# Kernel optimization log

Hardware: AMD Instinct MI355X
Metric: run time of the kernel (lower is better)

Reference implementation:

```python
import jax, jax.numpy as jnp
import numpy as np

L = 5  # history window (init kwarg)

def _mlp(x, W1, b1, W2, b2, W3, b3):
    h = jax.nn.relu(x @ W1 + b1)
    h = jax.nn.relu(h @ W2 + b2)
    return h @ W3 + b3

def setup_inputs() -> dict:
    key = jax.random.key(0)
    ks = jax.random.split(key, 12)
    N, T1, S, D, H, E = 2000, 11, 5, 64, 256, 100000
    IN = 2 * D + 2 * L * S + 3 + 1 + 1  # 183
    return {
        "features": jax.random.normal(ks[0], (N, D), jnp.float32),
        "states": jax.random.uniform(ks[1], (N, T1, S), jnp.float32),
        "distances": jax.random.uniform(ks[2], (N, N), jnp.float32),
        "W1": jax.random.normal(ks[3], (IN, H), jnp.float32) * 0.05,
        "b1": jnp.zeros((H,), jnp.float32),
        "W2": jax.random.normal(ks[4], (H, H), jnp.float32) * 0.05,
        "b2": jnp.zeros((H,), jnp.float32),
        "W3": jax.random.normal(ks[5], (H, 3), jnp.float32) * 0.05,
        "b3": jnp.zeros((3,), jnp.float32),
        "pairs_i": jax.random.randint(ks[6], (E,), 0, N, jnp.int32),
        "pairs_j": jax.random.randint(ks[7], (E,), 0, N, jnp.int32),
        "max_timestep": 10,
    }

def reference(features, states, distances, W1, b1, W2, b2, W3, b3, pairs_i, pairs_j, max_timestep):
    T = int(max_timestep)  # static
    N, T1, S = states.shape
    E = pairs_i.shape[0]
    # --- state histories: hist[t, n] = states[n, max(0,t-L+1)..t] zero-padded, flattened to L*S
    pad = jnp.pad(states, ((0, 0), (L - 1, 0), (0, 0)))  # [N, T1+L-1, S]
    idx = jnp.arange(T + 1)[:, None] + jnp.arange(L)[None, :]  # [T+1, L]
    hist = pad[:, idx, :]  # [N, T+1, L, S]
    hist = jnp.transpose(hist, (1, 0, 2, 3)).reshape(T + 1, N, L * S)
    hist = jax.lax.stop_gradient(hist)  # original .detach()

    fi = features[pairs_i]              # [E, D]
    fj = features[pairs_j]              # [E, D]
    dist = distances[pairs_i, pairs_j][:, None]  # [E, 1]
    eye3 = jnp.eye(3, dtype=features.dtype)

    # --- t = 0: is_initial=1, dummy prev type = onehot(0); same conditional for all k_prev
    x0 = jnp.concatenate([
        fi, fj, hist[0, pairs_i], hist[0, pairs_j],
        jnp.broadcast_to(eye3[0], (E, 3)), dist, jnp.ones_like(dist)
    ], axis=-1)
    p0 = jax.nn.softmax(_mlp(x0, W1, b1, W2, b2, W3, b3), axis=-1)  # [E, 3]
    cond0 = jnp.broadcast_to(p0[:, None, :], (E, 3, 3))              # [E, 3, 3]
    m0 = p0

    # --- t >= 1: one NN call on 3 stacked prev-type branches, then forward-algo recursion
    hp_i = hist[1:, pairs_i]  # [T, E, L*S]
    hp_j = hist[1:, pairs_j]
    prev3 = jnp.broadcast_to(eye3[:, None, :], (3, E, 3))
    tail = jnp.concatenate([dist, jnp.zeros_like(dist)], axis=-1)  # [E, 2] (dist, is_initial=0)

    def step(m_prev, xs):
        hi, hj = xs
        base = jnp.concatenate([fi, fj, hi, hj], axis=-1)  # [E, 2D+2LS]
        x = jnp.concatenate([
            jnp.broadcast_to(base[None], (3, E, base.shape[-1])),
            prev3,
            jnp.broadcast_to(tail[None], (3, E, 2)),
        ], axis=-1)  # [3, E, IN]
        probs = jax.nn.softmax(_mlp(x, W1, b1, W2, b2, W3, b3), axis=-1)  # [3, E, 3]
        cond = jnp.transpose(probs, (1, 0, 2))  # [E, k_prev, k_next]
        m = jnp.einsum('ek,ekn->en', m_prev, cond)
        return m, (cond, m)

    _, (conds, margs) = jax.lax.scan(step, m0, (hp_i, hp_j))
    conditionals = jnp.concatenate([cond0[None], conds], axis=0)  # [T+1, E, 3, 3]
    marginals = jnp.concatenate([m0[None], margs], axis=0)        # [T+1, E, 3]
    return conditionals, marginals
```

## Files before the change

kernel.cpp:

```cpp
#include <hip/hip_runtime.h>
#include <hip/hip_bf16.h>
#include <math.h>

#define D_F   64
#define IN_F  183
#define KS1   6
#define KS2   8
#define HID   256
#define HPITCH 264
#define BM    64
#define BLK   512

typedef unsigned short u16;
typedef __attribute__((ext_vector_type(8))) short bf16x8;
typedef __attribute__((ext_vector_type(4))) float f32x4;

__device__ __forceinline__ u16 f2bf(float v) {
    __hip_bfloat16 h = __float2bfloat16(v);
    u16 u; __builtin_memcpy(&u, &h, 2); return u;
}

__global__ void pack_w_kernel(const float* __restrict__ W, u16* __restrict__ Wp,
                              int K, int KSs)
{
    int g = blockIdx.x * 256 + threadIdx.x;
    int total = 16 * KSs * 64;
    if (g >= total) return;
    int lane = g & 63;
    int ks   = (g >> 6) % KSs;
    int mt   = (g >> 6) / KSs;
    int col  = mt * 16 + (lane & 15);
    int kb   = ks * 32 + 8 * (lane >> 4);
    u16 out[8];
    #pragma unroll
    for (int j = 0; j < 8; ++j) {
        int k = kb + j;
        out[j] = f2bf((k < K) ? W[(size_t)k * HID + col] : 0.0f);
    }
    *(bf16x8*)(Wp + (size_t)g * 8) = *(const bf16x8*)out;
}

__global__ void pack_w3_kernel(const float* __restrict__ W3, u16* __restrict__ W3p)
{
    int g = blockIdx.x * 256 + threadIdx.x;
    if (g >= KS2 * 64) return;
    int lane = g & 63;
    int ks   = g >> 6;
    int n    = lane & 15;
    int kb   = ks * 32 + 8 * (lane >> 4);
    u16 out[8];
    #pragma unroll
    for (int j = 0; j < 8; ++j)
        out[j] = f2bf((n < 3) ? W3[(size_t)(kb + j) * 3 + n] : 0.0f);
    *(bf16x8*)(W3p + (size_t)g * 8) = *(const bf16x8*)out;
}

__global__ __launch_bounds__(BLK)
void mfp_mlp_mfma(const float* __restrict__ features,
                  const float* __restrict__ states,
                  const float* __restrict__ distances,
                  const float* __restrict__ W1,
                  const u16* __restrict__ W1p, const float* __restrict__ b1,
                  const u16* __restrict__ W2p, const float* __restrict__ b2,
                  const u16* __restrict__ W3p, const float* __restrict__ b3,
                  const int* __restrict__ pairs_i, const int* __restrict__ pairs_j,
                  float* __restrict__ cond,
                  int N, int T1s, int E, int T)
{
    extern __shared__ char smem[];
    u16* buf0 = (u16*)smem;
    u16* buf1 = buf0 + BM * HPITCH;
    u16* hsB  = buf1 + BM * HPITCH;
    __shared__ int   s_pi[BM], s_pj[BM], s_e[BM], s_val[BM];
    __shared__ float s_dist[BM];

    const int tid = threadIdx.x;
    const int t   = blockIdx.y;
    const int nk  = (t == 0) ? 1 : 3;

    if (tid < BM) {
        int pe = blockIdx.x * BM + tid;
        int valid = (pe < E) ? 1 : 0;
        int e = valid ? pe : 0;
        int pi = pairs_i[e], pj = pairs_j[e];
        s_e[tid] = e; s_val[tid] = valid; s_pi[tid] = pi; s_pj[tid] = pj;
        s_dist[tid] = distances[(long long)pi * N + pj];
    }
    __syncthreads();

    u16* xs = buf0;
    for (int idx = tid; idx < BM * 32; idx += BLK) {
        int m = idx >> 5;
        int q = idx & 31;
        int src = (q < 16) ? s_pi[m] : s_pj[m];
        int c4  = (q & 15) * 4;
        float4 f = *(const float4*)&features[(size_t)src * D_F + c4];
        int c = ((q < 16) ? 0 : 64) + c4;
        ushort4 o;
        o.x = f2bf(f.x); o.y = f2bf(f.y); o.z = f2bf(f.z); o.w = f2bf(f.w);
        *(ushort4*)(xs + m * HPITCH + c) = o;
    }
    for (int idx = tid; idx < BM * 64; idx += BLK) {
        int m = idx >> 6;
        int c = 128 + (idx & 63);
        float v;
        if (c < 178) {
            int cc = c - 128;
            int row = (cc < 25) ? s_pi[m] : s_pj[m];
            int c2  = (cc < 25) ? cc : (cc - 25);
            int l = c2 / 5;
            int s = c2 - l * 5;
            int tau = t - 4 + l;
            v = (tau >= 0) ? states[((size_t)row * T1s + tau) * 5 + s] : 0.0f;
        } else if (c == 181) {
            v = s_dist[m];
        } else if (c == 182) {
            v = (t == 0) ? 1.0f : 0.0f;
        } else {
            v = 0.0f;
        }
        xs[m * HPITCH + c] = f2bf(v);
    }
    __syncthreads();

    const int lane = tid & 63;
    const int w    = tid >> 6;
    const int lr   = lane & 15;
    const int lg   = lane >> 4;

    f32x4 acc1[2][4];
    #pragma unroll
    for (int a = 0; a < 2; ++a)
        #pragma unroll
        for (int b = 0; b < 4; ++b)
            acc1[a][b] = (f32x4){0.f, 0.f, 0.f, 0.f};

    for (int ks = 0; ks < KS1; ++ks) {
        bf16x8 wfr[2];
        #pragma unroll
        for (int mtl = 0; mtl < 2; ++mtl)
            wfr[mtl] = *(const bf16x8*)(W1p + (((size_t)(2 * w + mtl) * KS1 + ks) * 64 + lane) * 8);
        bf16x8 xfr[4];
        #pragma unroll
        for (int nt = 0; nt < 4; ++nt)
            xfr[nt] = *(const bf16x8*)(xs + (nt * 16 + lr) * HPITCH + ks * 32 + 8 * lg);
        #pragma unroll
        for (int mtl = 0; mtl < 2; ++mtl)
            #pragma unroll
            for (int nt = 0; nt < 4; ++nt)
                acc1[mtl][nt] = __builtin_amdgcn_mfma_f32_16x16x32_bf16(wfr[mtl], xfr[nt], acc1[mtl][nt], 0, 0, 0);
    }

    f32x4 b1q[2], b2q[2];
    #pragma unroll
    for (int mtl = 0; mtl < 2; ++mtl) {
        int h0 = 16 * (2 * w + mtl) + 4 * lg;
        b1q[mtl] = *(const f32x4*)&b1[h0];
        b2q[mtl] = *(const f32x4*)&b2[h0];
    }
    const float b30 = b3[0], b31 = b3[1], b32 = b3[2];

    __syncthreads();

    #pragma unroll
    for (int mtl = 0; mtl < 2; ++mtl) {
        int h0 = 16 * (2 * w + mtl) + 4 * lg;
        f32x4 ohq = *(const f32x4*)&W1[(size_t)178 * HID + h0];
        #pragma unroll
        for (int nt = 0; nt < 4; ++nt) {
            ushort4 p;
            p.x = f2bf(fmaxf(acc1[mtl][nt][0] + b1q[mtl][0] + ohq[0], 0.0f));
            p.y = f2bf(fmaxf(acc1[mtl][nt][1] + b1q[mtl][1] + ohq[1], 0.0f));
            p.z = f2bf(fmaxf(acc1[mtl][nt][2] + b1q[mtl][2] + ohq[2], 0.0f));
            p.w = f2bf(fmaxf(acc1[mtl][nt][3] + b1q[mtl][3] + ohq[3], 0.0f));
            *(ushort4*)(buf1 + (nt * 16 + lr) * HPITCH + h0) = p;
        }
    }
    __syncthreads();

    for (int k = 0; k < nk; ++k) {
        u16* cur = (k & 1) ? buf0 : buf1;
        u16* nxt = (k & 1) ? buf1 : buf0;

        if (k + 1 < nk) {
            #pragma unroll
            for (int mtl = 0; mtl < 2; ++mtl) {
                int h0 = 16 * (2 * w + mtl) + 4 * lg;
                f32x4 ohq = *(const f32x4*)&W1[(size_t)(178 + k + 1) * HID + h0];
                #pragma unroll
                for (int nt = 0; nt < 4; ++nt) {
                    ushort4 p;
                    p.x = f2bf(fmaxf(acc1[mtl][nt][0] + b1q[mtl][0] + ohq[0], 0.0f));
                    p.y = f2bf(fmaxf(acc1[mtl][nt][1] + b1q[mtl][1] + ohq[1], 0.0f));
                    p.z = f2bf(fmaxf(acc1[mtl][nt][2] + b1q[mtl][2] + ohq[2], 0.0f));
                    p.w = f2bf(fmaxf(acc1[mtl][nt][3] + b1q[mtl][3] + ohq[3], 0.0f));
                    *(ushort4*)(nxt + (nt * 16 + lr) * HPITCH + h0) = p;
                }
            }
        }

        f32x4 acc2[2][4];
        #pragma unroll
        for (int a = 0; a < 2; ++a)
            #pragma unroll
            for (int b = 0; b < 4; ++b)
                acc2[a][b] = (f32x4){0.f, 0.f, 0.f, 0.f};

        for (int ks = 0; ks < KS2; ++ks) {
            bf16x8 wfr[2];
            #pragma unroll
            for (int mtl = 0; mtl < 2; ++mtl)
                wfr[mtl] = *(const bf16x8*)(W2p + (((size_t)(2 * w + mtl) * KS2 + ks) * 64 + lane) * 8);
            bf16x8 hfr[4];
            #pragma unroll
            for (int nt = 0; nt < 4; ++nt)
                hfr[nt] = *(const bf16x8*)(cur + (nt * 16 + lr) * HPITCH + ks * 32 + 8 * lg);
            #pragma unroll
            for (int mtl = 0; mtl < 2; ++mtl)
                #pragma unroll
                for (int nt = 0; nt < 4; ++nt)
                    acc2[mtl][nt] = __builtin_amdgcn_mfma_f32_16x16x32_bf16(wfr[mtl], hfr[nt], acc2[mtl][nt], 0, 0, 0);
        }

        #pragma unroll
        for (int mtl = 0; mtl < 2; ++mtl) {
            int h0 = 16 * (2 * w + mtl) + 4 * lg;
            #pragma unroll
            for (int nt = 0; nt < 4; ++nt) {
                ushort4 p;
                p.x = f2bf(fmaxf(acc2[mtl][nt][0] + b2q[mtl][0], 0.0f));
                p.y = f2bf(fmaxf(acc2[mtl][nt][1] + b2q[mtl][1], 0.0f));
                p.z = f2bf(fmaxf(acc2[mtl][nt][2] + b2q[mtl][2], 0.0f));
                p.w = f2bf(fmaxf(acc2[mtl][nt][3] + b2q[mtl][3], 0.0f));
                *(ushort4*)(hsB + (nt * 16 + lr) * HPITCH + h0) = p;
            }
        }
        __syncthreads();

        if (w < 4) {
            f32x4 acc3 = (f32x4){0.f, 0.f, 0.f, 0.f};
            for (int ks = 0; ks < KS2; ++ks) {
                bf16x8 hfr = *(const bf16x8*)(hsB + (w * 16 + lr) * HPITCH + ks * 32 + 8 * lg);
                bf16x8 wfr = *(const bf16x8*)(W3p + ((size_t)(ks * 64 + lane)) * 8);
                acc3 = __builtin_amdgcn_mfma_f32_16x16x32_bf16(wfr, hfr, acc3, 0, 0, 0);
            }
            int m = 16 * w + lr;
            if (lg == 0 && s_val[m]) {
                float l0 = acc3[0] + b30;
                float l1 = acc3[1] + b31;
                float l2 = acc3[2] + b32;
                float mx = fmaxf(l0, fmaxf(l1, l2));
                float e0 = expf(l0 - mx), e1 = expf(l1 - mx), e2 = expf(l2 - mx);
                float inv = 1.0f / (e0 + e1 + e2);
                float p0 = e0 * inv, p1 = e1 * inv, p2 = e2 * inv;
                size_t base = ((size_t)t * E + s_e[m]) * 9;
                if (t == 0) {
                    #pragma unroll
                    for (int kb = 0; kb < 3; ++kb) {
                        cond[base + kb * 3 + 0] = p0;
                        cond[base + kb * 3 + 1] = p1;
                        cond[base + kb * 3 + 2] = p2;
                    }
                } else {
                    cond[base + k * 3 + 0] = p0;
                    cond[base + k * 3 + 1] = p1;
                    cond[base + k * 3 + 2] = p2;
                }
            }
        }
        __syncthreads();
    }
}

__global__ __launch_bounds__(256)
void mfp_marg_kernel(const float* __restrict__ cond,
                     float* __restrict__ marg,
                     int E, int T)
{
    int e = blockIdx.x * 256 + threadIdx.x;
    if (e >= E) return;
    const float* c0 = &cond[(size_t)e * 9];
    float m0 = c0[0], m1 = c0[1], m2 = c0[2];
    marg[(size_t)e * 3 + 0] = m0;
    marg[(size_t)e * 3 + 1] = m1;
    marg[(size_t)e * 3 + 2] = m2;
    for (int t = 1; t <= T; ++t) {
        const float* c9 = &cond[((size_t)t * E + e) * 9];
        float n0 = m0 * c9[0] + m1 * c9[3] + m2 * c9[6];
        float n1 = m0 * c9[1] + m1 * c9[4] + m2 * c9[7];
        float n2 = m0 * c9[2] + m1 * c9[5] + m2 * c9[8];
        m0 = n0; m1 = n1; m2 = n2;
        float* mo = &marg[((size_t)t * E + e) * 3];
        mo[0] = m0; mo[1] = m1; mo[2] = m2;
    }
}

extern "C" void kernel_launch(void* const* d_in, const int* in_sizes, int n_in,
                              void* d_out, int out_size, void* d_ws, size_t ws_size,
                              hipStream_t stream) {
    const float* features  = (const float*)d_in[0];
    const float* states    = (const float*)d_in[1];
    const float* distances = (const float*)d_in[2];
    const float* W1 = (const float*)d_in[3];
    const float* b1 = (const float*)d_in[4];
    const float* W2 = (const float*)d_in[5];
    const float* b2 = (const float*)d_in[6];
    const float* W3 = (const float*)d_in[7];
    const float* b3 = (const float*)d_in[8];
    const int* pairs_i = (const int*)d_in[9];
    const int* pairs_j = (const int*)d_in[10];

    const int N   = in_sizes[0] / D_F;
    const int T1s = in_sizes[1] / (N * 5);
    const int E   = in_sizes[9];
    const int T   = out_size / (12 * E) - 1;

    float* cond = (float*)d_out;
    float* marg = (float*)d_out + (size_t)(T + 1) * E * 9;

    u16* W1p = (u16*)d_ws;
    u16* W2p = W1p + 16 * KS1 * 64 * 8;
    u16* W3p = W2p + 16 * KS2 * 64 * 8;

    {
        int g1 = 16 * KS1 * 64;
        int g2 = 16 * KS2 * 64;
        int g3 = KS2 * 64;
        pack_w_kernel<<<(g1 + 255) / 256, 256, 0, stream>>>(W1, W1p, IN_F, KS1);
        pack_w_kernel<<<(g2 + 255) / 256, 256, 0, stream>>>(W2, W2p, HID, KS2);
        pack_w3_kernel<<<(g3 + 255) / 256, 256, 0, stream>>>(W3, W3p);
    }

    dim3 grid((E + BM - 1) / BM, T + 1);
    const size_t lds_bytes = (size_t)3 * BM * HPITCH * sizeof(u16);

    mfp_mlp_mfma<<<grid, BLK, lds_bytes, stream>>>(
        features, states, distances, W1, W1p, b1, W2p, b2, W3p, b3,
        pairs_i, pairs_j, cond, N, T1s, E, T);

    mfp_marg_kernel<<<(E + 255) / 256, 256, 0, stream>>>(cond, marg, E, T);
}
```

Baseline: 868.8 us.

## Precompute per-node feature projections and loop timesteps inside each block

```diff
diff --git a/kernel.cpp b/kernel.cpp
--- a/kernel.cpp
+++ b/kernel.cpp
@@ -8,6 +8,7 @@
 #define KS2   8
 #define HID   256
 #define HPITCH 264
+#define XP2   72
 #define BM    64
 #define BLK   512
 
@@ -55,14 +56,44 @@
     *(bf16x8*)(W3p + (size_t)g * 8) = *(const bf16x8*)out;
 }
 
+__global__ __launch_bounds__(256)
+void a1_kernel(const float* __restrict__ features, const float* __restrict__ W1,
+               float* __restrict__ A1, int N)
+{
+    const int side = blockIdx.y;
+    const int n0   = blockIdx.x * 16;
+    const int h    = threadIdx.x;
+    __shared__ float sf[16][D_F];
+    for (int idx = threadIdx.x; idx < 16 * D_F; idx += 256) {
+        int ni = idx >> 6, d = idx & 63;
+        int n = n0 + ni;
+        sf[ni][d] = (n < N) ? features[(size_t)n * D_F + d] : 0.0f;
+    }
+    __syncthreads();
+    float acc[16];
+    #pragma unroll
+    for (int ni = 0; ni < 16; ++ni) acc[ni] = 0.0f;
+    for (int d = 0; d < D_F; ++d) {
+        float wv = W1[(size_t)(side * D_F + d) * HID + h];
+        #pragma unroll
+        for (int ni = 0; ni < 16; ++ni)
+            acc[ni] = fmaf(sf[ni][d], wv, acc[ni]);
+    }
+    #pragma unroll
+    for (int ni = 0; ni < 16; ++ni) {
+        int n = n0 + ni;
+        if (n < N) A1[((size_t)side * N + n) * HID + h] = acc[ni];
+    }
+}
+
 __global__ __launch_bounds__(BLK)
-void mfp_mlp_mfma(const float* __restrict__ features,
-                  const float* __restrict__ states,
+void mfp_mlp_mfma(const float* __restrict__ states,
                   const float* __restrict__ distances,
                   const float* __restrict__ W1,
                   const u16* __restrict__ W1p, const float* __restrict__ b1,
                   const u16* __restrict__ W2p, const float* __restrict__ b2,
                   const u16* __restrict__ W3p, const float* __restrict__ b3,
+                  const float* __restrict__ A1,
                   const int* __restrict__ pairs_i, const int* __restrict__ pairs_j,
                   float* __restrict__ cond,
                   int N, int T1s, int E, int T)
@@ -71,12 +102,13 @@
     u16* buf0 = (u16*)smem;
     u16* buf1 = buf0 + BM * HPITCH;
     u16* hsB  = buf1 + BM * HPITCH;
+    u16* x2   = hsB  + BM * HPITCH;
     __shared__ int   s_pi[BM], s_pj[BM], s_e[BM], s_val[BM];
     __shared__ float s_dist[BM];
 
-    const int tid = threadIdx.x;
-    const int t   = blockIdx.y;
-    const int nk  = (t == 0) ? 1 : 3;
+    const int tid  = threadIdx.x;
+    const int tbeg = blockIdx.y ? 6 : 0;
+    const int tend = blockIdx.y ? 11 : 6;
 
     if (tid < BM) {
         int pe = blockIdx.x * BM + tid;
@@ -88,69 +120,11 @@
     }
     __syncthreads();
 
-    u16* xs = buf0;
-    for (int idx = tid; idx < BM * 32; idx += BLK) {
-        int m = idx >> 5;
-        int q = idx & 31;
-        int src = (q < 16) ? s_pi[m] : s_pj[m];
-        int c4  = (q & 15) * 4;
-        float4 f = *(const float4*)&features[(size_t)src * D_F + c4];
-        int c = ((q < 16) ? 0 : 64) + c4;
-        ushort4 o;
-        o.x = f2bf(f.x); o.y = f2bf(f.y); o.z = f2bf(f.z); o.w = f2bf(f.w);
-        *(ushort4*)(xs + m * HPITCH + c) = o;
-    }
-    for (int idx = tid; idx < BM * 64; idx += BLK) {
-        int m = idx >> 6;
-        int c = 128 + (idx & 63);
-        float v;
-        if (c < 178) {
-            int cc = c - 128;
-            int row = (cc < 25) ? s_pi[m] : s_pj[m];
-            int c2  = (cc < 25) ? cc : (cc - 25);
-            int l = c2 / 5;
-            int s = c2 - l * 5;
-            int tau = t - 4 + l;
-            v = (tau >= 0) ? states[((size_t)row * T1s + tau) * 5 + s] : 0.0f;
-        } else if (c == 181) {
-            v = s_dist[m];
-        } else if (c == 182) {
-            v = (t == 0) ? 1.0f : 0.0f;
-        } else {
-            v = 0.0f;
-        }
-        xs[m * HPITCH + c] = f2bf(v);
-    }
-    __syncthreads();
-
     const int lane = tid & 63;
     const int w    = tid >> 6;
     const int lr   = lane & 15;
     const int lg   = lane >> 4;
 
-    f32x4 acc1[2][4];
-    #pragma unroll
-    for (int a = 0; a < 2; ++a)
-        #pragma unroll
-        for (int b = 0; b < 4; ++b)
-            acc1[a][b] = (f32x4){0.f, 0.f, 0.f, 0.f};
-
-    for (int ks = 0; ks < KS1; ++ks) {
-        bf16x8 wfr[2];
-        #pragma unroll
-        for (int mtl = 0; mtl < 2; ++mtl)
-            wfr[mtl] = *(const bf16x8*)(W1p + (((size_t)(2 * w + mtl) * KS1 + ks) * 64 + lane) * 8);
-        bf16x8 xfr[4];
-        #pragma unroll
-        for (int nt = 0; nt < 4; ++nt)
-            xfr[nt] = *(const bf16x8*)(xs + (nt * 16 + lr) * HPITCH + ks * 32 + 8 * lg);
-        #pragma unroll
-        for (int mtl = 0; mtl < 2; ++mtl)
-            #pragma unroll
-            for (int nt = 0; nt < 4; ++nt)
-                acc1[mtl][nt] = __builtin_amdgcn_mfma_f32_16x16x32_bf16(wfr[mtl], xfr[nt], acc1[mtl][nt], 0, 0, 0);
-    }
-
     f32x4 b1q[2], b2q[2];
     #pragma unroll
     for (int mtl = 0; mtl < 2; ++mtl) {
@@ -160,115 +134,168 @@
     }
     const float b30 = b3[0], b31 = b3[1], b32 = b3[2];
 
-    __syncthreads();
-
-    #pragma unroll
-    for (int mtl = 0; mtl < 2; ++mtl) {
-        int h0 = 16 * (2 * w + mtl) + 4 * lg;
-        f32x4 ohq = *(const f32x4*)&W1[(size_t)178 * HID + h0];
-        #pragma unroll
-        for (int nt = 0; nt < 4; ++nt) {
-            ushort4 p;
-            p.x = f2bf(fmaxf(acc1[mtl][nt][0] + b1q[mtl][0] + ohq[0], 0.0f));
-            p.y = f2bf(fmaxf(acc1[mtl][nt][1] + b1q[mtl][1] + ohq[1], 0.0f));
-            p.z = f2bf(fmaxf(acc1[mtl][nt][2] + b1q[mtl][2] + ohq[2], 0.0f));
-            p.w = f2bf(fmaxf(acc1[mtl][nt][3] + b1q[mtl][3] + ohq[3], 0.0f));
-            *(ushort4*)(buf1 + (nt * 16 + lr) * HPITCH + h0) = p;
-        }
-    }
-    __syncthreads();
-
-    for (int k = 0; k < nk; ++k) {
-        u16* cur = (k & 1) ? buf0 : buf1;
-        u16* nxt = (k & 1) ? buf1 : buf0;
-
-        if (k + 1 < nk) {
-            #pragma unroll
-            for (int mtl = 0; mtl < 2; ++mtl) {
-                int h0 = 16 * (2 * w + mtl) + 4 * lg;
-                f32x4 ohq = *(const f32x4*)&W1[(size_t)(178 + k + 1) * HID + h0];
-                #pragma unroll
-                for (int nt = 0; nt < 4; ++nt) {
-                    ushort4 p;
-                    p.x = f2bf(fmaxf(acc1[mtl][nt][0] + b1q[mtl][0] + ohq[0], 0.0f));
-                    p.y = f2bf(fmaxf(acc1[mtl][nt][1] + b1q[mtl][1] + ohq[1], 0.0f));
-                    p.z = f2bf(fmaxf(acc1[mtl][nt][2] + b1q[mtl][2] + ohq[2], 0.0f));
-                    p.w = f2bf(fmaxf(acc1[mtl][nt][3] + b1q[mtl][3] + ohq[3], 0.0f));
-                    *(ushort4*)(nxt + (nt * 16 + lr) * HPITCH + h0) = p;
-                }
-            }
-        }
-
-        f32x4 acc2[2][4];
-        #pragma unroll
-        for (int a = 0; a < 2; ++a)
-            #pragma unroll
-            for (int b = 0; b < 4; ++b)
-                acc2[a][b] = (f32x4){0.f, 0.f, 0.f, 0.f};
-
-        for (int ks = 0; ks < KS2; ++ks) {
-            bf16x8 wfr[2];
-            #pragma unroll
-            for (int mtl = 0; mtl < 2; ++mtl)
-                wfr[mtl] = *(const bf16x8*)(W2p + (((size_t)(2 * w + mtl) * KS2 + ks) * 64 + lane) * 8);
-            bf16x8 hfr[4];
-            #pragma unroll
-            for (int nt = 0; nt < 4; ++nt)
-                hfr[nt] = *(const bf16x8*)(cur + (nt * 16 + lr) * HPITCH + ks * 32 + 8 * lg);
-            #pragma unroll
-            for (int mtl = 0; mtl < 2; ++mtl)
-                #pragma unroll
-                for (int nt = 0; nt < 4; ++nt)
-                    acc2[mtl][nt] = __builtin_amdgcn_mfma_f32_16x16x32_bf16(wfr[mtl], hfr[nt], acc2[mtl][nt], 0, 0, 0);
-        }
-
+    for (int t = tbeg; t < tend && t <= T; ++t) {
+        const int nk = (t == 0) ? 1 : 3;
+
+        for (int idx = tid; idx < BM * 64; idx += BLK) {
+            int m  = idx >> 6;
+            int c2 = idx & 63;
+            float v;
+            if (c2 < 50) {
+                int row = (c2 < 25) ? s_pi[m] : s_pj[m];
+                int cc  = (c2 < 25) ? c2 : (c2 - 25);
+                int l = cc / 5;
+                int s = cc - l * 5;
+                int tau = t - 4 + l;
+                v = (tau >= 0) ? states[((size_t)row * T1s + tau) * 5 + s] : 0.0f;
+            } else if (c2 == 53) {
+                v = s_dist[m];
+            } else if (c2 == 54) {
+                v = (t == 0) ? 1.0f : 0.0f;
+            } else {
+                v = 0.0f;
+            }
+            x2[m * XP2 + c2] = f2bf(v);
+        }
+
+        f32x4 acc1[2][4];
         #pragma unroll
         for (int mtl = 0; mtl < 2; ++mtl) {
             int h0 = 16 * (2 * w + mtl) + 4 * lg;
             #pragma unroll
             for (int nt = 0; nt < 4; ++nt) {
+                int m = 16 * nt + lr;
+                f32x4 qa = *(const f32x4*)&A1[((size_t)s_pi[m]) * HID + h0];
+                f32x4 qb = *(const f32x4*)&A1[((size_t)N + s_pj[m]) * HID + h0];
+                acc1[mtl][nt] = qa + qb;
+            }
+        }
+        __syncthreads();
+
+        for (int ks = 4; ks < 6; ++ks) {
+            bf16x8 wfr[2];
+            #pragma unroll
+            for (int mtl = 0; mtl < 2; ++mtl)
+                wfr[mtl] = *(const bf16x8*)(W1p + (((size_t)(2 * w + mtl) * KS1 + ks) * 64 + lane) * 8);
+            bf16x8 xfr[4];
+            #pragma unroll
+            for (int nt = 0; nt < 4; ++nt)
+                xfr[nt] = *(const bf16x8*)(x2 + (16 * nt + lr) * XP2 + (ks - 4) * 32 + 8 * lg);
+            #pragma unroll
+            for (int mtl = 0; mtl < 2; ++mtl)
+                #pragma unroll
+                for (int nt = 0; nt < 4; ++nt)
+                    acc1[mtl][nt] = __builtin_amdgcn_mfma_f32_16x16x32_bf16(wfr[mtl], xfr[nt], acc1[mtl][nt], 0, 0, 0);
+        }
+
+        #pragma unroll
+        for (int mtl = 0; mtl < 2; ++mtl) {
+            int h0 = 16 * (2 * w + mtl) + 4 * lg;
+            f32x4 ohq = *(const f32x4*)&W1[(size_t)178 * HID + h0];
+            #pragma unroll
+            for (int nt = 0; nt < 4; ++nt) {
                 ushort4 p;
-                p.x = f2bf(fmaxf(acc2[mtl][nt][0] + b2q[mtl][0], 0.0f));
-                p.y = f2bf(fmaxf(acc2[mtl][nt][1] + b2q[mtl][1], 0.0f));
-                p.z = f2bf(fmaxf(acc2[mtl][nt][2] + b2q[mtl][2], 0.0f));
-                p.w = f2bf(fmaxf(acc2[mtl][nt][3] + b2q[mtl][3], 0.0f));
-                *(ushort4*)(hsB + (nt * 16 + lr) * HPITCH + h0) = p;
+                p.x = f2bf(fmaxf(acc1[mtl][nt][0] + b1q[mtl][0] + ohq[0], 0.0f));
+                p.y = f2bf(fmaxf(acc1[mtl][nt][1] + b1q[mtl][1] + ohq[1], 0.0f));
+                p.z = f2bf(fmaxf(acc1[mtl][nt][2] + b1q[mtl][2] + ohq[2], 0.0f));
+                p.w = f2bf(fmaxf(acc1[mtl][nt][3] + b1q[mtl][3] + ohq[3], 0.0f));
+                *(ushort4*)(buf1 + (nt * 16 + lr) * HPITCH + h0) = p;
             }
         }
         __syncthreads();
 
-        if (w < 4) {
-            f32x4 acc3 = (f32x4){0.f, 0.f, 0.f, 0.f};
+        for (int k = 0; k < nk; ++k) {
+            u16* cur = (k & 1) ? buf0 : buf1;
+            u16* nxt = (k & 1) ? buf1 : buf0;
+
+            if (k + 1 < nk) {
+                #pragma unroll
+                for (int mtl = 0; mtl < 2; ++mtl) {
+                    int h0 = 16 * (2 * w + mtl) + 4 * lg;
+                    f32x4 ohq = *(const f32x4*)&W1[(size_t)(178 + k + 1) * HID + h0];
+                    #pragma unroll
+                    for (int nt = 0; nt < 4; ++nt) {
+                        ushort4 p;
+                        p.x = f2bf(fmaxf(acc1[mtl][nt][0] + b1q[mtl][0] + ohq[0], 0.0f));
+                        p.y = f2bf(fmaxf(acc1[mtl][nt][1] + b1q[mtl][1] + ohq[1], 0.0f));
+                        p.z = f2bf(fmaxf(acc1[mtl][nt][2] + b1q[mtl][2] + ohq[2], 0.0f));
+                        p.w = f2bf(fmaxf(acc1[mtl][nt][3] + b1q[mtl][3] + ohq[3], 0.0f));
+                        *(ushort4*)(nxt + (nt * 16 + lr) * HPITCH + h0) = p;
+                    }
+                }
+            }
+
+            f32x4 acc2[2][4];
+            #pragma unroll
+            for (int a = 0; a < 2; ++a)
+                #pragma unroll
+                for (int b = 0; b < 4; ++b)
+                    acc2[a][b] = (f32x4){0.f, 0.f, 0.f, 0.f};
+
             for (int ks = 0; ks < KS2; ++ks) {
-                bf16x8 hfr = *(const bf16x8*)(hsB + (w * 16 + lr) * HPITCH + ks * 32 + 8 * lg);
-                bf16x8 wfr = *(const bf16x8*)(W3p + ((size_t)(ks * 64 + lane)) * 8);
-                acc3 = __builtin_amdgcn_mfma_f32_16x16x32_bf16(wfr, hfr, acc3, 0, 0, 0);
-            }
-            int m = 16 * w + lr;
-            if (lg == 0 && s_val[m]) {
-                float l0 = acc3[0] + b30;
-                float l1 = acc3[1] + b31;
-                float l2 = acc3[2] + b32;
-                float mx = fmaxf(l0, fmaxf(l1, l2));
-                float e0 = expf(l0 - mx), e1 = expf(l1 - mx), e2 = expf(l2 - mx);
-                float inv = 1.0f / (e0 + e1 + e2);
-                float p0 = e0 * inv, p1 = e1 * inv, p2 = e2 * inv;
-                size_t base = ((size_t)t * E + s_e[m]) * 9;
-                if (t == 0) {
+                bf16x8 wfr[2];
+                #pragma unroll
+                for (int mtl = 0; mtl < 2; ++mtl)
+                    wfr[mtl] = *(const bf16x8*)(W2p + (((size_t)(2 * w + mtl) * KS2 + ks) * 64 + lane) * 8);
+                bf16x8 hfr[4];
+                #pragma unroll
+                for (int nt = 0; nt < 4; ++nt)
+                    hfr[nt] = *(const bf16x8*)(cur + (nt * 16 + lr) * HPITCH + ks * 32 + 8 * lg);
+                #pragma unroll
+                for (int mtl = 0; mtl < 2; ++mtl)
                     #pragma unroll
-                    for (int kb = 0; kb < 3; ++kb) {
-                        cond[base + kb * 3 + 0] = p0;
-                        cond[base + kb * 3 + 1] = p1;
-                        cond[base + kb * 3 + 2] = p2;
+                    for (int nt = 0; nt < 4; ++nt)
+                        acc2[mtl][nt] = __builtin_amdgcn_mfma_f32_16x16x32_bf16(wfr[mtl], hfr[nt], acc2[mtl][nt], 0, 0, 0);
+            }
+
+            #pragma unroll
+            for (int mtl = 0; mtl < 2; ++mtl) {
+                int h0 = 16 * (2 * w + mtl) + 4 * lg;
+                #pragma unroll
+                for (int nt = 0; nt < 4; ++nt) {
+                    ushort4 p;
+                    p.x = f2bf(fmaxf(acc2[mtl][nt][0] + b2q[mtl][0], 0.0f));
+                    p.y = f2bf(fmaxf(acc2[mtl][nt][1] + b2q[mtl][1], 0.0f));
+                    p.z = f2bf(fmaxf(acc2[mtl][nt][2] + b2q[mtl][2], 0.0f));
+                    p.w = f2bf(fmaxf(acc2[mtl][nt][3] + b2q[mtl][3], 0.0f));
+                    *(ushort4*)(hsB + (nt * 16 + lr) * HPITCH + h0) = p;
+                }
+            }
+            __syncthreads();
+
+            if (w < 4) {
+                f32x4 acc3 = (f32x4){0.f, 0.f, 0.f, 0.f};
+                for (int ks = 0; ks < KS2; ++ks) {
+                    bf16x8 hfr = *(const bf16x8*)(hsB + (w * 16 + lr) * HPITCH + ks * 32 + 8 * lg);
+                    bf16x8 wfr = *(const bf16x8*)(W3p + ((size_t)(ks * 64 + lane)) * 8);
+                    acc3 = __builtin_amdgcn_mfma_f32_16x16x32_bf16(wfr, hfr, acc3, 0, 0, 0);
+                }
+                int m = 16 * w + lr;
+                if (lg == 0 && s_val[m]) {
+                    float l0 = acc3[0] + b30;
+                    float l1 = acc3[1] + b31;
+                    float l2 = acc3[2] + b32;
+                    float mx = fmaxf(l0, fmaxf(l1, l2));
+                    float e0 = expf(l0 - mx), e1 = expf(l1 - mx), e2 = expf(l2 - mx);
+                    float inv = 1.0f / (e0 + e1 + e2);
+                    float p0 = e0 * inv, p1 = e1 * inv, p2 = e2 * inv;
+                    size_t base = ((size_t)t * E + s_e[m]) * 9;
+                    if (t == 0) {
+                        #pragma unroll
+                        for (int kb = 0; kb < 3; ++kb) {
+                            cond[base + kb * 3 + 0] = p0;
+                            cond[base + kb * 3 + 1] = p1;
+                            cond[base + kb * 3 + 2] = p2;
+                        }
+                    } else {
+                        cond[base + k * 3 + 0] = p0;
+                        cond[base + k * 3 + 1] = p1;
+                        cond[base + k * 3 + 2] = p2;
                     }
-                } else {
-                    cond[base + k * 3 + 0] = p0;
-                    cond[base + k * 3 + 1] = p1;
-                    cond[base + k * 3 + 2] = p2;
                 }
             }
-        }
-        __syncthreads();
+            __syncthreads();
+        }
     }
 }
 
@@ -317,6 +344,7 @@
 
     float* cond = (float*)d_out;
     float* marg = (float*)d_out + (size_t)(T + 1) * E * 9;
+    float* A1   = marg;
 
     u16* W1p = (u16*)d_ws;
     u16* W2p = W1p + 16 * KS1 * 64 * 8;
@@ -329,13 +357,16 @@
         pack_w_kernel<<<(g1 + 255) / 256, 256, 0, stream>>>(W1, W1p, IN_F, KS1);
         pack_w_kernel<<<(g2 + 255) / 256, 256, 0, stream>>>(W2, W2p, HID, KS2);
         pack_w3_kernel<<<(g3 + 255) / 256, 256, 0, stream>>>(W3, W3p);
-    }
-
-    dim3 grid((E + BM - 1) / BM, T + 1);
-    const size_t lds_bytes = (size_t)3 * BM * HPITCH * sizeof(u16);
+        dim3 ga((N + 15) / 16, 2);
+        a1_kernel<<<ga, 256, 0, stream>>>(features, W1, A1, N);
+    }
+
+    dim3 grid((E + BM - 1) / BM, 2);
+    const size_t lds_bytes = (size_t)3 * BM * HPITCH * sizeof(u16)
+                           + (size_t)BM * XP2 * sizeof(u16);
 
     mfp_mlp_mfma<<<grid, BLK, lds_bytes, stream>>>(
-        features, states, distances, W1, W1p, b1, W2p, b2, W3p, b3,
+        states, distances, W1, W1p, b1, W2p, b2, W3p, b3, A1,
         pairs_i, pairs_j, cond, N, T1s, E, T);
 
     mfp_marg_kernel<<<(E + 255) / 256, 256, 0, stream>>>(cond, marg, E, T);
```

New measurement: 957.8 us. 10.2% more time.
